# Optimization experiments

Hardware: AMD Instinct MI355X
Metric: run time of the kernel (lower is better)

Reference implementation:

```python
import jax, jax.numpy as jnp
import numpy as np

N_NODES = 20000
N_USERS = 100000
N_PRODUCTS = 10000
D = 128
N_EDGES = 640000
N_LAYERS = 2


def gcn_conv(x, W, b, edge_index, num_nodes):
    """PyG-style GCNConv: add self-loops, symmetric degree norm, scatter-add."""
    h = x @ W  # [N, D]
    loop = jnp.arange(num_nodes, dtype=edge_index.dtype)
    src = jnp.concatenate([edge_index[0], loop])
    dst = jnp.concatenate([edge_index[1], loop])
    deg = jax.ops.segment_sum(jnp.ones_like(dst, dtype=h.dtype), dst,
                              num_segments=num_nodes)
    dinv = jnp.where(deg > 0, jax.lax.rsqrt(deg), 0.0)
    norm = dinv[src] * dinv[dst]  # [E+N]
    msg = norm[:, None] * h[src]  # gather + scale
    out = jax.ops.segment_sum(msg, dst, num_segments=num_nodes)  # scatter-add
    return out + b


def setup_inputs() -> dict:
    key = jax.random.key(0)
    ks = jax.random.split(key, 12)
    s = 0.05
    return {
        "user_ids": jax.random.randint(ks[0], (N_NODES,), 0, N_USERS),
        "product_ids": jax.random.randint(ks[1], (N_NODES,), 0, N_PRODUCTS),
        "edge_index_user": jax.random.randint(ks[2], (2, N_EDGES), 0, N_NODES),
        "edge_index_product": jax.random.randint(ks[3], (2, N_EDGES), 0, N_NODES),
        "user_emb_table": jax.random.normal(ks[4], (N_USERS, D), jnp.float32),
        "product_emb_table": jax.random.normal(ks[5], (N_PRODUCTS, D), jnp.float32),
        "user_conv_W": jax.random.normal(ks[6], (N_LAYERS, D, D), jnp.float32) * s,
        "user_conv_b": jnp.zeros((N_LAYERS, D), jnp.float32),
        "product_conv_W": jax.random.normal(ks[7], (N_LAYERS, D, D), jnp.float32) * s,
        "product_conv_b": jnp.zeros((N_LAYERS, D), jnp.float32),
        "out_W": jax.random.normal(ks[8], (2 * D, N_PRODUCTS), jnp.float32) * s,
        "out_b": jnp.zeros((N_PRODUCTS,), jnp.float32),
    }


def reference(user_ids, product_ids, edge_index_user, edge_index_product,
              user_emb_table, product_emb_table,
              user_conv_W, user_conv_b, product_conv_W, product_conv_b,
              out_W, out_b):
    u = user_emb_table[user_ids]       # [N, D]
    p = product_emb_table[product_ids]  # [N, D]
    for i in range(N_LAYERS):
        # dropout is identity in eval mode
        u = gcn_conv(u, user_conv_W[i], user_conv_b[i], edge_index_user, N_NODES)
        p = gcn_conv(p, product_conv_W[i], product_conv_b[i], edge_index_product, N_NODES)
    combined = jnp.concatenate([u, p], axis=1)  # [N, 2D]
    logits = combined @ out_W + out_b           # [N, n_products]
    return jax.nn.softmax(logits, axis=1)
```

## Files before the change

### kernel.cpp

```cpp
#include <hip/hip_runtime.h>
#include <cstdint>
#include <cstddef>

#define NN 20000
#define NE 640000
#define DD 128
#define NP 10000
#define NRT 1250
#define NRT_PAD 1256
#define NCT_PAD 632
#define NWG_BIG 474

typedef __attribute__((ext_vector_type(8))) short short8;
typedef __attribute__((ext_vector_type(4))) float f32x4;

static __device__ __forceinline__ unsigned short f2bf(float f){
  uint32_t u = __float_as_uint(f);
  return (unsigned short)((u + 0x7fffu + ((u >> 16) & 1u)) >> 16);
}
static __device__ __forceinline__ float bf2f(unsigned short u){
  return __uint_as_float(((uint32_t)u) << 16);
}

static __device__ __forceinline__ void gload_lds16(const void* g, void* l){
  __builtin_amdgcn_global_load_lds(
      (const __attribute__((address_space(1))) void*)g,
      (__attribute__((address_space(3))) void*)l, 16, 0, 0);
}

#define PREP_NWG 7784
__global__ __launch_bounds__(256) void k_prep(
    const int* __restrict__ dst_u, const int* __restrict__ dst_p, int* __restrict__ cnt,
    const float* __restrict__ uW, const float* __restrict__ pW,
    unsigned short* __restrict__ WuF0, unsigned short* __restrict__ WuF1,
    unsigned short* __restrict__ WpF0, unsigned short* __restrict__ WpF1,
    const float* __restrict__ oW, unsigned short* __restrict__ WoF){
  __shared__ float tile[32][33];
  const int b = blockIdx.x, tid = threadIdx.x;

  if (b < 5000){
    int i = b * 256 + tid;
    if (i < NE) atomicAdd(&cnt[dst_u[i]], 1);
    else atomicAdd(&cnt[NN + dst_p[i - NE]], 1);

  } else if (b < 5256){
    int bw = b - 5000;
    int wy = bw >> 6, bx = bw & 63;
    const float* W; unsigned short* Wf;
    switch (wy){
      case 0: W = uW;                   Wf = WuF0; break;
      case 1: W = uW + (size_t)DD * DD; Wf = WuF1; break;
      case 2: W = pW;                   Wf = WpF0; break;
      default:W = pW + (size_t)DD * DD; Wf = WpF1; break;
    }
    int i = bx * 256 + tid;
    int e = i & 7, l = (i >> 3) & 63, rem = i >> 9;
    int kt = rem & 3, ct = rem >> 2;
    int col = ct * 16 + (l & 15);
    int k = kt * 32 + (l >> 4) * 8 + e;
    Wf[i] = f2bf(W[(size_t)k * DD + col]);

  } else {
    int bw = b - 5256;
    int bx = bw % 316, by = bw / 316;
    const int kb = by * 32, cb = bx * 32;
    const int tx = tid & 31, ty = tid >> 5;
    const int col = cb + tx;
    #pragma unroll
    for (int j = 0; j < 4; j++){
      int k = ty + j * 8;
      tile[k][tx] = (col < NP) ? oW[(size_t)(kb + k) * NP + col] : 0.f;
    }
    __syncthreads();
    const int ct2 = tid >> 7, rep = tid & 1, l = (tid >> 1) & 63;
    const int c_loc = ct2 * 16 + (l & 15);
    const int k_loc = (l >> 4) * 8 + rep * 4;
    ushort4 o;
    o.x = f2bf(tile[k_loc + 0][c_loc]);
    o.y = f2bf(tile[k_loc + 1][c_loc]);
    o.z = f2bf(tile[k_loc + 2][c_loc]);
    o.w = f2bf(tile[k_loc + 3][c_loc]);
    const int ct = cb / 16 + ct2, kt = kb / 32;
    *reinterpret_cast<ushort4*>(WoF + ((size_t)(ct * 8 + kt) * 64 + l) * 8 + rep * 4) = o;
  }
}

__global__ void k_scan2(const int* __restrict__ cnt, int* __restrict__ row_off,
                        int* __restrict__ cursor, float* __restrict__ dinv){
  __shared__ int part[1024];
  const int g = blockIdx.x;
  const int* c = cnt + g * NN;
  int* ro = row_off + g * (NN + 1);
  int* cur = cursor + g * NN;
  float* dv = dinv + g * NN;
  int t = threadIdx.x;
  int per = (NN + 1023) >> 10;
  int base = t * per;
  int s = 0;
  for (int i = 0; i < per; i++){
    int idx = base + i;
    if (idx < NN){
      int cv = c[idx];
      dv[idx] = rsqrtf((float)(cv + 1));
      s += cv;
    }
  }
  part[t] = s;
  __syncthreads();
  for (int off = 1; off < 1024; off <<= 1){
    int v = (t >= off) ? part[t - off] : 0;
    __syncthreads();
    part[t] += v;
    __syncthreads();
  }
  int run = (t == 0) ? 0 : part[t - 1];
  for (int i = 0; i < per; i++){
    int idx = base + i;
    if (idx < NN){ ro[idx] = run; cur[idx] = run; run += c[idx]; }
  }
  if (t == 0) ro[NN] = part[1023];
}

__global__ void k_fill2(const int* __restrict__ src_u, const int* __restrict__ dst_u,
                        const int* __restrict__ src_p, const int* __restrict__ dst_p,
                        int* __restrict__ cursor, int* __restrict__ col){
  int i = blockIdx.x * blockDim.x + threadIdx.x;
  if (i < NE){
    int p = atomicAdd(&cursor[dst_u[i]], 1);
    col[p] = src_u[i];
  } else if (i < 2 * NE){
    int j = i - NE;
    int p = atomicAdd(&cursor[NN + dst_p[j]], 1);
    col[NE + p] = src_p[j];
  }
}

__global__ __launch_bounds__(256) void k_l1(
    const float* __restrict__ utab, const int* __restrict__ uids,
    const float* __restrict__ ptab, const int* __restrict__ pids,
    const unsigned short* __restrict__ Wu, const unsigned short* __restrict__ Wp,
    const float* __restrict__ du, const float* __restrict__ dp,
    unsigned short* __restrict__ hu, unsigned short* __restrict__ hp){
  __shared__ unsigned short af[4 * 4 * 64 * 8];
  const int g = blockIdx.y;
  const float* tab = g ? ptab : utab;
  const int*   ids = g ? pids : uids;
  const unsigned short* Wf = g ? Wp : Wu;
  const float* dinv = g ? dp : du;
  unsigned short* hsb = g ? hp : hu;

  const int tid = threadIdx.x;
  const int tx = tid & 31, ny = tid >> 5;
  const int nbase = blockIdx.x * 64;
  #pragma unroll
  for (int rep = 0; rep < 8; rep++){
    int nl = ny + rep * 8;
    int node = nbase + nl;
    int id = ids[min(node, NN - 1)];
    const float4 v = *reinterpret_cast<const float4*>(tab + (size_t)id * DD + tx * 4);
    ushort4 o; o.x = f2bf(v.x); o.y = f2bf(v.y); o.z = f2bf(v.z); o.w = f2bf(v.w);
    int chunk = ((nl >> 4) * 4 + (tx >> 3)) * 64 + ((tx >> 1) & 3) * 16 + (nl & 15);
    *reinterpret_cast<ushort4*>(af + chunk * 8 + (tx & 1) * 4) = o;
  }
  __syncthreads();

  const int wid = tid >> 6, lane = tid & 63;
  const int gw = blockIdx.x * 4 + wid;
  const bool valid = gw < NRT;
  short8 a[4];
  #pragma unroll
  for (int kt = 0; kt < 4; kt++)
    a[kt] = *reinterpret_cast<const short8*>(af + ((wid * 4 + kt) * 64 + lane) * 8);
  const int fr = lane & 15, fq = lane >> 4;
  #pragma unroll
  for (int ct = 0; ct < 8; ct++){
    f32x4 acc = {0.f, 0.f, 0.f, 0.f};
    #pragma unroll
    for (int kt = 0; kt < 4; kt++){
      short8 b = *reinterpret_cast<const short8*>(Wf + ((size_t)(ct * 4 + kt) * 64 + lane) * 8);
      acc = __builtin_amdgcn_mfma_f32_16x16x32_bf16(a[kt], b, acc, 0, 0, 0);
    }
    if (valid){
      #pragma unroll
      for (int r = 0; r < 4; r++){
        int grow = gw * 16 + fq * 4 + r;
        hsb[(size_t)grow * DD + ct * 16 + fr] = f2bf(dinv[grow] * acc[r]);
      }
    }
  }
}

__global__ __launch_bounds__(256) void k_l2(
    const unsigned short* __restrict__ hu, const unsigned short* __restrict__ hp,
    const float* __restrict__ du, const float* __restrict__ dp,
    const int* __restrict__ ro, const int* __restrict__ colb,
    const float* __restrict__ bu, const float* __restrict__ bp,
    const unsigned short* __restrict__ Wu, const unsigned short* __restrict__ Wp,
    unsigned short* __restrict__ hu2, unsigned short* __restrict__ hp2){
  __shared__ unsigned short af[4 * 4 * 64 * 8];
  const int g = blockIdx.y;
  const unsigned short* hin = g ? hp : hu;
  const float* dv   = g ? dp : du;
  const float* bias = g ? bp : bu;
  const unsigned short* Wf = g ? Wp : Wu;
  unsigned short* hout = g ? hp2 : hu2;
  const int* row_off = ro + g * (NN + 1);
  const int* col     = colb + (size_t)g * NE;

  const int tid = threadIdx.x;
  const int tx = tid & 15, nsub = tid >> 4;
  const short8* h8 = reinterpret_cast<const short8*>(hin);
  for (int s = 0; s < 4; s++){
    const int nl = s * 16 + nsub;
    const int node = blockIdx.x * 64 + nl;
    if (node < NN){
      float a[8];
      {
        short8 v = h8[(size_t)node * 16 + tx];
        #pragma unroll
        for (int j = 0; j < 8; j++) a[j] = bf2f((unsigned short)v[j]);
      }
      int st = row_off[node], e = row_off[node + 1];
      int i = st;
      for (; i + 3 < e; i += 4){
        short8 v0 = h8[(size_t)col[i] * 16 + tx];
        short8 v1 = h8[(size_t)col[i + 1] * 16 + tx];
        short8 v2 = h8[(size_t)col[i + 2] * 16 + tx];
        short8 v3 = h8[(size_t)col[i + 3] * 16 + tx];
        #pragma unroll
        for (int j = 0; j < 8; j++)
          a[j] += (bf2f((unsigned short)v0[j]) + bf2f((unsigned short)v1[j]))
                + (bf2f((unsigned short)v2[j]) + bf2f((unsigned short)v3[j]));
      }
      for (; i < e; i++){
        short8 v = h8[(size_t)col[i] * 16 + tx];
        #pragma unroll
        for (int j = 0; j < 8; j++) a[j] += bf2f((unsigned short)v[j]);
      }
      const float dn = dv[node];
      short8 ov;
      #pragma unroll
      for (int j = 0; j < 8; j++)
        ov[j] = (short)f2bf(dn * a[j] + bias[tx * 8 + j]);
      int chunk = (s * 4 + (tx >> 2)) * 64 + (tx & 3) * 16 + (nl & 15);
      *reinterpret_cast<short8*>(af + chunk * 8) = ov;
    }
  }
  __syncthreads();

  const int wid = tid >> 6, lane = tid & 63;
  const int gw = blockIdx.x * 4 + wid;
  const bool valid = gw < NRT;
  short8 a[4];
  #pragma unroll
  for (int kt = 0; kt < 4; kt++)
    a[kt] = *reinterpret_cast<const short8*>(af + ((wid * 4 + kt) * 64 + lane) * 8);
  const int fr = lane & 15, fq = lane >> 4;
  #pragma unroll
  for (int ct = 0; ct < 8; ct++){
    f32x4 acc = {0.f, 0.f, 0.f, 0.f};
    #pragma unroll
    for (int kt = 0; kt < 4; kt++){
      short8 b = *reinterpret_cast<const short8*>(Wf + ((size_t)(ct * 4 + kt) * 64 + lane) * 8);
      acc = __builtin_amdgcn_mfma_f32_16x16x32_bf16(a[kt], b, acc, 0, 0, 0);
    }
    if (valid){
      #pragma unroll
      for (int r = 0; r < 4; r++){
        int grow = gw * 16 + fq * 4 + r;
        hout[(size_t)grow * DD + ct * 16 + fr] = f2bf(dv[grow] * acc[r]);
      }
    }
  }
}

__global__ void k_agg2(const unsigned short* __restrict__ hu, const unsigned short* __restrict__ hp,
                       const float* __restrict__ du, const float* __restrict__ dp,
                       const int* __restrict__ ro, const int* __restrict__ colb,
                       const float* __restrict__ bu, const float* __restrict__ bp,
                       unsigned short* __restrict__ xfu, unsigned short* __restrict__ xfp,
                       int KT, int toff_p){
  const int g = blockIdx.y;
  const unsigned short* hsb = g ? hp : hu;
  const float* dv   = g ? dp : du;
  const float* bias = g ? bp : bu;
  unsigned short* xf = g ? xfp : xfu;
  const int* row_off = ro + g * (NN + 1);
  const int* col     = colb + (size_t)g * NE;
  const int toff = g ? toff_p : 0;

  int node = blockIdx.x * blockDim.y + threadIdx.y;
  int tx = threadIdx.x;
  if (node >= NN) return;
  const short8* h8 = reinterpret_cast<const short8*>(hsb);
  float a[8];
  {
    short8 v = h8[(size_t)node * 16 + tx];
    #pragma unroll
    for (int j = 0; j < 8; j++) a[j] = bf2f((unsigned short)v[j]);
  }
  int s = row_off[node], e = row_off[node + 1];
  int i = s;
  for (; i + 3 < e; i += 4){
    short8 v0 = h8[(size_t)col[i] * 16 + tx];
    short8 v1 = h8[(size_t)col[i + 1] * 16 + tx];
    short8 v2 = h8[(size_t)col[i + 2] * 16 + tx];
    short8 v3 = h8[(size_t)col[i + 3] * 16 + tx];
    #pragma unroll
    for (int j = 0; j < 8; j++)
      a[j] += (bf2f((unsigned short)v0[j]) + bf2f((unsigned short)v1[j]))
            + (bf2f((unsigned short)v2[j]) + bf2f((unsigned short)v3[j]));
  }
  for (; i < e; i++){
    short8 v = h8[(size_t)col[i] * 16 + tx];
    #pragma unroll
    for (int j = 0; j < 8; j++) a[j] += bf2f((unsigned short)v[j]);
  }
  float dn = dv[node];
  short8 ov;
  #pragma unroll
  for (int j = 0; j < 8; j++)
    ov[j] = (short)f2bf(dn * a[j] + bias[tx * 8 + j]);
  size_t chunk = ((size_t)(node >> 4) * KT + toff + (tx >> 2)) * 64 + (tx & 3) * 16 + (node & 15);
  *reinterpret_cast<short8*>(xf + chunk * 8) = ov;
}

template<int PASS>
__global__ __launch_bounds__(256, 2) void k_big(
    const unsigned short* __restrict__ Af, const unsigned short* __restrict__ Bf,
    const float* __restrict__ ob, float* __restrict__ rowsum, float* __restrict__ out){
  __shared__ unsigned short sA[2][16384];
  const int tid = threadIdx.x, lane = tid & 63, wid = tid >> 6;
  const int wm = wid >> 1, wn = wid & 1;
  const int fr = lane & 15, fq = lane >> 4;

  const int orig = blockIdx.x;
  const int xcd = orig & 7, pos = orig >> 3;
  const int wgid = (xcd < 2 ? xcd * 60 : 120 + (xcd - 2) * 59) + pos;
  const int six = wgid / 79, cp = wgid - six * 79;
  const int rt0 = six * 52 + (six < 2 ? six : 2);
  const int nrt = 52 + (six < 2 ? 1 : 0);
  const int bct = cp * 8;

  short8 breg[4][8];
  #pragma unroll
  for (int n = 0; n < 4; n++)
    #pragma unroll
    for (int kt = 0; kt < 8; kt++)
      breg[n][kt] = *reinterpret_cast<const short8*>(
          Bf + (((size_t)(bct + wn * 4 + n) * 8 + kt) * 64 + lane) * 8);

  float obv[4];
  #pragma unroll
  for (int n = 0; n < 4; n++){
    int gcol = cp * 128 + wn * 64 + n * 16 + fr;
    obv[n] = (gcol < NP) ? ob[gcol] : 0.f;
  }

#define STAGEA(buf, rt) do{                                                    \
    _Pragma("unroll")                                                          \
    for (int i_ = 0; i_ < 8; i_++){                                            \
      int c_ = i_ * 256 + tid;                                                 \
      gload_lds16(Af + ((size_t)(rt) * 2048 + c_) * 8, (void*)&sA[buf][c_ * 8]); \
    } }while(0)

  STAGEA(0, rt0);
  for (int t = 0; t < nrt; t++){
    const int p = t & 1;
    if (t + 1 < nrt){
      STAGEA(p ^ 1, rt0 + t + 1);
      asm volatile("s_waitcnt vmcnt(8)" ::: "memory");
    } else {
      asm volatile("s_waitcnt vmcnt(0)" ::: "memory");
    }
    __builtin_amdgcn_s_barrier();

    f32x4 acc[2][4] = {};
    __builtin_amdgcn_s_setprio(1);
    #pragma unroll
    for (int m = 0; m < 2; m++)
      #pragma unroll
      for (int kt = 0; kt < 8; kt++){
        short8 a = *reinterpret_cast<const short8*>(
            &sA[p][(((wm * 2 + m) * 8 + kt) * 64 + lane) * 8]);
        #pragma unroll
        for (int n = 0; n < 4; n++)
          acc[m][n] = __builtin_amdgcn_mfma_f32_16x16x32_bf16(a, breg[n][kt], acc[m][n], 0, 0, 0);
      }
    __builtin_amdgcn_s_setprio(0);
    __builtin_amdgcn_s_barrier();

    const int rbase = (rt0 + t) * 64 + wm * 32;
    if (PASS == 0){
      #pragma unroll
      for (int m = 0; m < 2; m++)
        #pragma unroll
        for (int r = 0; r < 4; r++){
          const int grow = rbase + m * 16 + fq * 4 + r;
          float rs = 0.f;
          #pragma unroll
          for (int n = 0; n < 4; n++){
            const int gcol = cp * 128 + wn * 64 + n * 16 + fr;
            rs += (gcol < NP) ? __expf(acc[m][n][r] + obv[n]) : 0.f;
          }
          rs += __shfl_xor(rs, 1, 64);
          rs += __shfl_xor(rs, 2, 64);
          rs += __shfl_xor(rs, 4, 64);
          rs += __shfl_xor(rs, 8, 64);
          if (fr == 0 && grow < NN) atomicAdd(&rowsum[grow], rs);
        }
    } else {
      #pragma unroll
      for (int m = 0; m < 2; m++)
        #pragma unroll
        for (int r = 0; r < 4; r++){
          const int grow = rbase + m * 16 + fq * 4 + r;
          const bool rv = grow < NN;
          const float ri = rv ? 1.f / rowsum[grow] : 0.f;
          #pragma unroll
          for (int n = 0; n < 4; n++){
            const int gcol = cp * 128 + wn * 64 + n * 16 + fr;
            if (rv && gcol < NP)
              __builtin_nontemporal_store(ri * __expf(acc[m][n][r] + obv[n]),
                                          &out[(size_t)grow * NP + gcol]);
          }
        }
    }
  }
#undef STAGEA
}

extern "C" void kernel_launch(void* const* d_in, const int* in_sizes, int n_in,
                              void* d_out, int out_size, void* d_ws, size_t ws_size,
                              hipStream_t stream){
  const int*   user_ids = (const int*)d_in[0];
  const int*   prod_ids = (const int*)d_in[1];
  const int*   ei_u     = (const int*)d_in[2];
  const int*   ei_p     = (const int*)d_in[3];
  const float* utab     = (const float*)d_in[4];
  const float* ptab     = (const float*)d_in[5];
  const float* uW       = (const float*)d_in[6];
  const float* ub       = (const float*)d_in[7];
  const float* pW       = (const float*)d_in[8];
  const float* pb       = (const float*)d_in[9];
  const float* oW       = (const float*)d_in[10];
  const float* ob       = (const float*)d_in[11];
  float* out = (float*)d_out;
  (void)in_sizes; (void)n_in; (void)out_size; (void)ws_size;

  char* w = (char*)d_ws;
  size_t off = 0;
  auto alloc = [&](size_t bytes)->void*{
    void* p = w + off; off += (bytes + 255) & ~(size_t)255; return p;
  };
  int*   cnt    = (int*)alloc(2 * NN * 4);
  float* rowsum = (float*)alloc(NN * 4);
  float* dinv   = (float*)alloc(2 * NN * 4);
  int*   ro     = (int*)alloc(2 * (NN + 1) * 4);
  int*   cur    = (int*)alloc(2 * NN * 4);
  int*   colb   = (int*)alloc((size_t)2 * NE * 4);
  unsigned short* comb_f= (unsigned short*)alloc((size_t)NRT_PAD * 8 * 64 * 8 * 2);
  unsigned short* hu    = (unsigned short*)alloc((size_t)NN * DD * 2);
  unsigned short* hp    = (unsigned short*)alloc((size_t)NN * DD * 2);
  unsigned short* hu2   = (unsigned short*)alloc((size_t)NN * DD * 2);
  unsigned short* hp2   = (unsigned short*)alloc((size_t)NN * DD * 2);
  unsigned short* WuF0 = (unsigned short*)alloc((size_t)DD * DD * 2);
  unsigned short* WuF1 = (unsigned short*)alloc((size_t)DD * DD * 2);
  unsigned short* WpF0 = (unsigned short*)alloc((size_t)DD * DD * 2);
  unsigned short* WpF1 = (unsigned short*)alloc((size_t)DD * DD * 2);
  unsigned short* WoF  = (unsigned short*)alloc((size_t)NCT_PAD * 8 * 64 * 8 * 2);

  hipMemsetAsync(cnt, 0, (2 * NN + NN) * 4, stream);
  hipMemsetAsync(comb_f + (size_t)NRT * 8 * 64 * 8, 0,
                 (size_t)(NRT_PAD - NRT) * 8 * 64 * 8 * 2, stream);

  const int* src_u = ei_u;  const int* dst_u = ei_u + NE;
  const int* src_p = ei_p;  const int* dst_p = ei_p + NE;

  k_prep<<<PREP_NWG, 256, 0, stream>>>(dst_u, dst_p, cnt,
                                       uW, pW, WuF0, WuF1, WpF0, WpF1, oW, WoF);
  k_scan2<<<2, 1024, 0, stream>>>(cnt, ro, cur, dinv);
  k_fill2<<<(2 * NE + 255) / 256, 256, 0, stream>>>(src_u, dst_u, src_p, dst_p, cur, colb);

  const int convGrid = (NRT + 3) / 4;

  k_l1<<<dim3(convGrid, 2), 256, 0, stream>>>(utab, user_ids, ptab, prod_ids,
                                              WuF0, WpF0, dinv, dinv + NN, hu, hp);
  k_l2<<<dim3(convGrid, 2), 256, 0, stream>>>(hu, hp, dinv, dinv + NN, ro, colb,
                                              ub, pb, WuF1, WpF1, hu2, hp2);
  dim3 aggBlk(16, 16);
  k_agg2<<<dim3((NN + 15) / 16, 2), aggBlk, 0, stream>>>(hu2, hp2, dinv, dinv + NN, ro, colb,
                                                         ub + DD, pb + DD, comb_f, comb_f, 8, 4);

  k_big<0><<<NWG_BIG, 256, 0, stream>>>(comb_f, WoF, ob, rowsum, out);
  k_big<1><<<NWG_BIG, 256, 0, stream>>>(comb_f, WoF, ob, rowsum, out);
}
```

Before: 720.7 us.

## Replace atomic rowsum pass with dedicated row-stationary softmax-denominator kernel

The first GEMM pass, which computed exp-sums and accumulated them with global atomics, is replaced by a new kernel. In it each wave keeps one 16-row A tile in registers and streams all of B through double-buffered LDS, summing exp values in registers. Each row sum is then written once with no atomics, and the rowsum memset is dropped. The risk is lower parallelism: 314 workgroups each make 158 sequential B passes, and every workgroup reads the whole B matrix, so L2 traffic rises.

```diff
diff --git a/kernel.cpp b/kernel.cpp
--- a/kernel.cpp
+++ b/kernel.cpp
@@ -325,10 +325,84 @@
   *reinterpret_cast<short8*>(xf + chunk * 8) = ov;
 }
 
-template<int PASS>
+__global__ __launch_bounds__(256, 2) void k_rsum(
+    const unsigned short* __restrict__ Af, const unsigned short* __restrict__ Bf,
+    const float* __restrict__ ob, float* __restrict__ rowsum){
+  __shared__ unsigned short sB[2][16384];
+  const int tid = threadIdx.x, lane = tid & 63, wid = tid >> 6;
+  const int fr = lane & 15, fq = lane >> 4;
+  const int rt16 = blockIdx.x * 4 + wid;
+
+  short8 a[8];
+  #pragma unroll
+  for (int kt = 0; kt < 8; kt++)
+    a[kt] = *reinterpret_cast<const short8*>(Af + (((size_t)rt16 * 8 + kt) * 64 + lane) * 8);
+
+  float rs[4] = {0.f, 0.f, 0.f, 0.f};
+
+#define STAGEB(buf, pc) do{                                                    \
+    _Pragma("unroll")                                                          \
+    for (int i_ = 0; i_ < 8; i_++){                                            \
+      int c_ = i_ * 256 + tid;                                                 \
+      gload_lds16(Bf + ((size_t)(pc) * 2048 + c_) * 8, (void*)&sB[buf][c_ * 8]); \
+    } }while(0)
+
+  STAGEB(0, 0);
+  for (int pc = 0; pc < 158; pc++){
+    const int p = pc & 1;
+    if (pc + 1 < 158){
+      STAGEB(p ^ 1, pc + 1);
+      asm volatile("s_waitcnt vmcnt(8)" ::: "memory");
+    } else {
+      asm volatile("s_waitcnt vmcnt(0)" ::: "memory");
+    }
+    __builtin_amdgcn_s_barrier();
+
+    f32x4 acc[4];
+    __builtin_amdgcn_s_setprio(1);
+    #pragma unroll
+    for (int n = 0; n < 4; n++){
+      acc[n] = (f32x4){0.f, 0.f, 0.f, 0.f};
+      #pragma unroll
+      for (int kt = 0; kt < 8; kt++){
+        short8 b = *reinterpret_cast<const short8*>(&sB[p][((n * 8 + kt) * 64 + lane) * 8]);
+        acc[n] = __builtin_amdgcn_mfma_f32_16x16x32_bf16(a[kt], b, acc[n], 0, 0, 0);
+      }
+    }
+    __builtin_amdgcn_s_setprio(0);
+    __builtin_amdgcn_s_barrier();
+
+    #pragma unroll
+    for (int n = 0; n < 4; n++){
+      const int gcol = pc * 64 + n * 16 + fr;
+      if (gcol < NP){
+        const float obv = ob[gcol];
+        #pragma unroll
+        for (int r = 0; r < 4; r++)
+          rs[r] += __expf(acc[n][r] + obv);
+      }
+    }
+  }
+#undef STAGEB
+
+  #pragma unroll
+  for (int r = 0; r < 4; r++){
+    float v = rs[r];
+    v += __shfl_xor(v, 1, 64);
+    v += __shfl_xor(v, 2, 64);
+    v += __shfl_xor(v, 4, 64);
+    v += __shfl_xor(v, 8, 64);
+    if (fr == 0){
+      int grow = rt16 * 16 + fq * 4 + r;
+      if (grow < NN) rowsum[grow] = v;
+    }
+  }
+}
+
 __global__ __launch_bounds__(256, 2) void k_big(
     const unsigned short* __restrict__ Af, const unsigned short* __restrict__ Bf,
-    const float* __restrict__ ob, float* __restrict__ rowsum, float* __restrict__ out){
+    const float* __restrict__ ob, const float* __restrict__ rowsum,
+    float* __restrict__ out){
   __shared__ unsigned short sA[2][16384];
   const int tid = threadIdx.x, lane = tid & 63, wid = tid >> 6;
   const int wm = wid >> 1, wn = wid & 1;
@@ -391,41 +465,21 @@
     __builtin_amdgcn_s_barrier();
 
     const int rbase = (rt0 + t) * 64 + wm * 32;
-    if (PASS == 0){
+    #pragma unroll
+    for (int m = 0; m < 2; m++)
       #pragma unroll
-      for (int m = 0; m < 2; m++)
+      for (int r = 0; r < 4; r++){
+        const int grow = rbase + m * 16 + fq * 4 + r;
+        const bool rv = grow < NN;
+        const float ri = rv ? 1.f / rowsum[grow] : 0.f;
         #pragma unroll
-        for (int r = 0; r < 4; r++){
-          const int grow = rbase + m * 16 + fq * 4 + r;
-          float rs = 0.f;
-          #pragma unroll
-          for (int n = 0; n < 4; n++){
-            const int gcol = cp * 128 + wn * 64 + n * 16 + fr;
-            rs += (gcol < NP) ? __expf(acc[m][n][r] + obv[n]) : 0.f;
-          }
-          rs += __shfl_xor(rs, 1, 64);
-          rs += __shfl_xor(rs, 2, 64);
-          rs += __shfl_xor(rs, 4, 64);
-          rs += __shfl_xor(rs, 8, 64);
-          if (fr == 0 && grow < NN) atomicAdd(&rowsum[grow], rs);
+        for (int n = 0; n < 4; n++){
+          const int gcol = cp * 128 + wn * 64 + n * 16 + fr;
+          if (rv && gcol < NP)
+            __builtin_nontemporal_store(ri * __expf(acc[m][n][r] + obv[n]),
+                                        &out[(size_t)grow * NP + gcol]);
         }
-    } else {
-      #pragma unroll
-      for (int m = 0; m < 2; m++)
-        #pragma unroll
-        for (int r = 0; r < 4; r++){
-          const int grow = rbase + m * 16 + fq * 4 + r;
-          const bool rv = grow < NN;
-          const float ri = rv ? 1.f / rowsum[grow] : 0.f;
-          #pragma unroll
-          for (int n = 0; n < 4; n++){
-            const int gcol = cp * 128 + wn * 64 + n * 16 + fr;
-            if (rv && gcol < NP)
-              __builtin_nontemporal_store(ri * __expf(acc[m][n][r] + obv[n]),
-                                          &out[(size_t)grow * NP + gcol]);
-          }
-        }
-    }
+      }
   }
 #undef STAGEA
 }
@@ -470,7 +524,7 @@
   unsigned short* WpF1 = (unsigned short*)alloc((size_t)DD * DD * 2);
   unsigned short* WoF  = (unsigned short*)alloc((size_t)NCT_PAD * 8 * 64 * 8 * 2);
 
-  hipMemsetAsync(cnt, 0, (2 * NN + NN) * 4, stream);
+  hipMemsetAsync(cnt, 0, 2 * NN * 4, stream);
   hipMemsetAsync(comb_f + (size_t)NRT * 8 * 64 * 8, 0,
                  (size_t)(NRT_PAD - NRT) * 8 * 64 * 8 * 2, stream);
 
@@ -492,6 +546,6 @@
   k_agg2<<<dim3((NN + 15) / 16, 2), aggBlk, 0, stream>>>(hu2, hp2, dinv, dinv + NN, ro, colb,
                                                          ub + DD, pb + DD, comb_f, comb_f, 8, 4);
 
-  k_big<0><<<NWG_BIG, 256, 0, stream>>>(comb_f, WoF, ob, rowsum, out);
-  k_big<1><<<NWG_BIG, 256, 0, stream>>>(comb_f, WoF, ob, rowsum, out);
-}
+  k_rsum<<<NRT_PAD / 4, 256, 0, stream>>>(comb_f, WoF, ob, rowsum);
+  k_big<<<NWG_BIG, 256, 0, stream>>>(comb_f, WoF, ob, rowsum, out);
+}
```

New measurement: 753.2 us. +4.5%, slower.
